# Optimization experiments

Measured on AMD Instinct MI355X. Metric: run time of the kernel, lower is better.

## Reference

```python
import jax, jax.numpy as jnp
import numpy as np

B, S, H, NH = 1, 2048, 2048, 32
HD = H // NH  # 64
DFF = 4 * H
EPS = 1e-5


def layer_norm(x, w, b):
    mu = jnp.mean(x, axis=-1, keepdims=True)
    var = jnp.var(x, axis=-1, keepdims=True)
    return (x - mu) * jax.lax.rsqrt(var + EPS) * w + b


def setup_inputs() -> dict:
    key = jax.random.key(0)
    ks = jax.random.split(key, 16)
    std = 0.02
    hidden_states = jax.random.normal(ks[0], (B, S, H), dtype=jnp.float32)
    # additive causal mask [1,1,S,S]
    causal = jnp.tril(jnp.ones((S, S), dtype=jnp.bool_))
    attention_mask = jnp.where(causal, 0.0, -1e9).astype(jnp.float32)[None, None]
    p = lambda k, shp: (jax.random.normal(k, shp, dtype=jnp.float32) * std)
    return {
        "hidden_states": hidden_states,
        "attention_mask": attention_mask,
        "ln1_w": jnp.ones((H,), jnp.float32), "ln1_b": jnp.zeros((H,), jnp.float32),
        "wq": p(ks[1], (H, H)), "bq": jnp.zeros((H,), jnp.float32),
        "wk": p(ks[2], (H, H)), "bk": jnp.zeros((H,), jnp.float32),
        "wv": p(ks[3], (H, H)), "bv": jnp.zeros((H,), jnp.float32),
        "wo": p(ks[4], (H, H)), "bo": jnp.zeros((H,), jnp.float32),
        "w1": p(ks[5], (H, DFF)), "b1": jnp.zeros((DFF,), jnp.float32),
        "w2": p(ks[6], (DFF, H)), "b2": jnp.zeros((H,), jnp.float32),
        "ln2_w": jnp.ones((H,), jnp.float32), "ln2_b": jnp.zeros((H,), jnp.float32),
    }


def reference(hidden_states, attention_mask, ln1_w, ln1_b, wq, bq, wk, bk, wv, bv,
              wo, bo, w1, b1, w2, b2, ln2_w, ln2_b):
    x = hidden_states
    # --- pre-norm attention ---
    residual = x
    h = layer_norm(x, ln1_w, ln1_b)
    scaling = HD ** -0.5
    q = (h @ wq + bq).reshape(B, S, NH, HD) * scaling
    k = (h @ wk + bk).reshape(B, S, NH, HD)
    v = (h @ wv + bv).reshape(B, S, NH, HD)
    scores = jnp.einsum('bqhd,bkhd->bhqk', q, k) + attention_mask
    p = jax.nn.softmax(scores, axis=-1)  # dropout is identity in eval
    attn = jnp.einsum('bhqk,bkhd->bqhd', p, v).reshape(B, S, H)
    attn = attn @ wo + bo
    x = residual + attn
    # --- pre-norm MLP ---
    residual = x
    h = layer_norm(x, ln2_w, ln2_b)
    h = jax.nn.gelu(h @ w1 + b1, approximate=False) @ w2 + b2
    return residual + h
```

## Files before the change

kernel.cpp:

```cpp
#include <hip/hip_runtime.h>
#include <math.h>

#define H 2048
#define S 2048
#define NH 32
#define HD 64
#define DFF 8192

typedef __attribute__((ext_vector_type(4))) float f32x4;
typedef __attribute__((ext_vector_type(8))) short short8;

static __device__ __forceinline__ ushort f2bf(float f) {
  unsigned u = __float_as_uint(f);
  u += 0x7fff + ((u >> 16) & 1);
  return (ushort)(u >> 16);
}

static __device__ __forceinline__ void gl_lds16(const ushort* g, ushort* l) {
  __builtin_amdgcn_global_load_lds(
      (__attribute__((address_space(1))) const void*)g,
      (__attribute__((address_space(3))) void*)l, 16, 0, 0);
}

__global__ __launch_bounds__(256) void transpose_cast_kernel(
    const float* __restrict__ W, ushort* __restrict__ Wt, int K, int N) {
  __shared__ __align__(16) ushort tile[64][72];
  int n0 = blockIdx.x * 64, k0 = blockIdx.y * 64;
  int t = threadIdx.x;
  int lk = t >> 4;
  int ln4 = (t & 15) * 4;
#pragma unroll
  for (int p = 0; p < 4; p++) {
    int k = p * 16 + lk;
    float4 v = *reinterpret_cast<const float4*>(&W[(size_t)(k0 + k) * N + n0 + ln4]);
    float vv[4] = {v.x, v.y, v.z, v.w};
#pragma unroll
    for (int i = 0; i < 4; i++) {
      int row = ln4 + i;
      int slot = ((k >> 3) ^ (row & 7));
      tile[row][(slot << 3) + (k & 7)] = f2bf(vv[i]);
    }
  }
  __syncthreads();
  int n = t >> 2;
  int kq = (t & 3) * 8;
#pragma unroll
  for (int p = 0; p < 2; p++) {
    int kk = kq + p * 32;
    int slot = ((kk >> 3) ^ (n & 7));
    short8 o = *reinterpret_cast<const short8*>(&tile[n][slot << 3]);
    *reinterpret_cast<short8*>(&Wt[(size_t)(n0 + n) * K + k0 + kk]) = o;
  }
}

__global__ __launch_bounds__(256) void vtrans_kernel(
    const ushort* __restrict__ V, ushort* __restrict__ VT) {
  __shared__ ushort tile[32][33];
  int s0 = blockIdx.x * 32, d0 = blockIdx.y * 32;
  int tx = threadIdx.x & 31, ty = threadIdx.x >> 5;
#pragma unroll
  for (int i = 0; i < 4; i++)
    tile[ty * 4 + i][tx] = V[(size_t)(s0 + ty * 4 + i) * H + d0 + tx];
  __syncthreads();
#pragma unroll
  for (int i = 0; i < 4; i++)
    VT[(size_t)(d0 + ty * 4 + i) * S + s0 + tx] = tile[tx][ty * 4 + i];
}

__global__ __launch_bounds__(256) void biascat_kernel(
    const float* __restrict__ bq, const float* __restrict__ bk,
    const float* __restrict__ bv, float* __restrict__ o) {
  int t = blockIdx.x * 256 + threadIdx.x;
  o[t] = (t < H) ? bq[t] : (t < 2 * H) ? bk[t - H] : bv[t - 2 * H];
}

__global__ __launch_bounds__(256) void ln_kernel(
    const float* __restrict__ x, const float* __restrict__ w,
    const float* __restrict__ b, ushort* __restrict__ out) {
  int row = blockIdx.x, t = threadIdx.x;
  const float4* xr = reinterpret_cast<const float4*>(x + (size_t)row * H);
  float4 v0 = xr[t * 2], v1 = xr[t * 2 + 1];
  float s = v0.x + v0.y + v0.z + v0.w + v1.x + v1.y + v1.z + v1.w;
  float q = v0.x * v0.x + v0.y * v0.y + v0.z * v0.z + v0.w * v0.w +
            v1.x * v1.x + v1.y * v1.y + v1.z * v1.z + v1.w * v1.w;
#pragma unroll
  for (int off = 32; off > 0; off >>= 1) {
    s += __shfl_down(s, off, 64);
    q += __shfl_down(q, off, 64);
  }
  __shared__ float sm[8];
  int lane = t & 63, wv = t >> 6;
  if (lane == 0) { sm[wv] = s; sm[wv + 4] = q; }
  __syncthreads();
  s = sm[0] + sm[1] + sm[2] + sm[3];
  q = sm[4] + sm[5] + sm[6] + sm[7];
  float mu = s * (1.0f / H);
  float var = q * (1.0f / H) - mu * mu;
  float rs = rsqrtf(var + 1e-5f);
  const float4* wr = reinterpret_cast<const float4*>(w);
  const float4* br = reinterpret_cast<const float4*>(b);
  float4 w0 = wr[t * 2], w1v = wr[t * 2 + 1], b0 = br[t * 2], b1v = br[t * 2 + 1];
  short8 pk;
  pk[0] = (short)f2bf((v0.x - mu) * rs * w0.x + b0.x);
  pk[1] = (short)f2bf((v0.y - mu) * rs * w0.y + b0.y);
  pk[2] = (short)f2bf((v0.z - mu) * rs * w0.z + b0.z);
  pk[3] = (short)f2bf((v0.w - mu) * rs * w0.w + b0.w);
  pk[4] = (short)f2bf((v1.x - mu) * rs * w1v.x + b1v.x);
  pk[5] = (short)f2bf((v1.y - mu) * rs * w1v.y + b1v.y);
  pk[6] = (short)f2bf((v1.z - mu) * rs * w1v.z + b1v.z);
  pk[7] = (short)f2bf((v1.w - mu) * rs * w1v.w + b1v.w);
  *reinterpret_cast<short8*>(out + (size_t)row * H + t * 8) = pk;
}

__global__ __launch_bounds__(256) void combine4_kernel(
    const float* __restrict__ res, const float* __restrict__ p0,
    const float* __restrict__ p1, const float* __restrict__ p2,
    const float* __restrict__ p3, const float* __restrict__ bias,
    float* __restrict__ out) {
  size_t i = (size_t)blockIdx.x * 256 + threadIdx.x;
  float4 a = reinterpret_cast<const float4*>(res)[i];
  float4 c0 = reinterpret_cast<const float4*>(p0)[i];
  float4 c1 = reinterpret_cast<const float4*>(p1)[i];
  float4 c2 = reinterpret_cast<const float4*>(p2)[i];
  float4 c3 = reinterpret_cast<const float4*>(p3)[i];
  int col = (int)((i * 4) & (H - 1));
  float4 bb = *reinterpret_cast<const float4*>(bias + col);
  float4 o;
  o.x = a.x + c0.x + c1.x + c2.x + c3.x + bb.x;
  o.y = a.y + c0.y + c1.y + c2.y + c3.y + bb.y;
  o.z = a.z + c0.z + c1.z + c2.z + c3.z + bb.z;
  o.w = a.w + c0.w + c1.w + c2.w + c3.w + bb.w;
  reinterpret_cast<float4*>(out)[i] = o;
}

__global__ __launch_bounds__(256) void combine_ln_kernel(
    const float* __restrict__ res, const float* __restrict__ p0,
    const float* __restrict__ p1, const float* __restrict__ bias,
    const float* __restrict__ lw, const float* __restrict__ lb,
    float* __restrict__ xout, ushort* __restrict__ lnout) {
  int row = blockIdx.x, t = threadIdx.x;
  const float4* rr = reinterpret_cast<const float4*>(res + (size_t)row * H);
  const float4* r0 = reinterpret_cast<const float4*>(p0 + (size_t)row * H);
  const float4* r1 = reinterpret_cast<const float4*>(p1 + (size_t)row * H);
  const float4* bb = reinterpret_cast<const float4*>(bias);
  float4 a0 = rr[t * 2], a1 = rr[t * 2 + 1];
  float4 c0 = r0[t * 2], c1 = r0[t * 2 + 1];
  float4 d0 = r1[t * 2], d1 = r1[t * 2 + 1];
  float4 e0 = bb[t * 2], e1 = bb[t * 2 + 1];
  float4 v0, v1;
  v0.x = a0.x + c0.x + d0.x + e0.x;
  v0.y = a0.y + c0.y + d0.y + e0.y;
  v0.z = a0.z + c0.z + d0.z + e0.z;
  v0.w = a0.w + c0.w + d0.w + e0.w;
  v1.x = a1.x + c1.x + d1.x + e1.x;
  v1.y = a1.y + c1.y + d1.y + e1.y;
  v1.z = a1.z + c1.z + d1.z + e1.z;
  v1.w = a1.w + c1.w + d1.w + e1.w;
  float4* xo = reinterpret_cast<float4*>(xout + (size_t)row * H);
  xo[t * 2] = v0;
  xo[t * 2 + 1] = v1;
  float s = v0.x + v0.y + v0.z + v0.w + v1.x + v1.y + v1.z + v1.w;
  float q = v0.x * v0.x + v0.y * v0.y + v0.z * v0.z + v0.w * v0.w +
            v1.x * v1.x + v1.y * v1.y + v1.z * v1.z + v1.w * v1.w;
#pragma unroll
  for (int off = 32; off > 0; off >>= 1) {
    s += __shfl_down(s, off, 64);
    q += __shfl_down(q, off, 64);
  }
  __shared__ float sm[8];
  int lane = t & 63, wv = t >> 6;
  if (lane == 0) { sm[wv] = s; sm[wv + 4] = q; }
  __syncthreads();
  s = sm[0] + sm[1] + sm[2] + sm[3];
  q = sm[4] + sm[5] + sm[6] + sm[7];
  float mu = s * (1.0f / H);
  float var = q * (1.0f / H) - mu * mu;
  float rs = rsqrtf(var + 1e-5f);
  const float4* wr = reinterpret_cast<const float4*>(lw);
  const float4* br = reinterpret_cast<const float4*>(lb);
  float4 w0 = wr[t * 2], w1v = wr[t * 2 + 1], b0 = br[t * 2], b1v = br[t * 2 + 1];
  short8 pk;
  pk[0] = (short)f2bf((v0.x - mu) * rs * w0.x + b0.x);
  pk[1] = (short)f2bf((v0.y - mu) * rs * w0.y + b0.y);
  pk[2] = (short)f2bf((v0.z - mu) * rs * w0.z + b0.z);
  pk[3] = (short)f2bf((v0.w - mu) * rs * w0.w + b0.w);
  pk[4] = (short)f2bf((v1.x - mu) * rs * w1v.x + b1v.x);
  pk[5] = (short)f2bf((v1.y - mu) * rs * w1v.y + b1v.y);
  pk[6] = (short)f2bf((v1.z - mu) * rs * w1v.z + b1v.z);
  pk[7] = (short)f2bf((v1.w - mu) * rs * w1v.w + b1v.w);
  *reinterpret_cast<short8*>(lnout + (size_t)row * H + t * 8) = pk;
}

template <int MODE>
__global__ __launch_bounds__(512, 2) void gemm256_kernel(
    const ushort* __restrict__ A, const ushort* __restrict__ Bt,
    const float* __restrict__ bias,
    ushort* __restrict__ outb, float* __restrict__ outf,
    int M, int N, int lda, int kbeg, int klen) {
  __shared__ __align__(16) ushort As[2][256 * 64];
  __shared__ __align__(16) ushort Bs[2][256 * 64];
  int tid = threadIdx.x, lane = tid & 63, w = tid >> 6;
  int lm = lane & 15, kg = lane >> 4;
  int wr = w >> 2, wc = w & 3;
  int gx = gridDim.x, nwg = gx * gridDim.y;
  int orig = blockIdx.y * gx + blockIdx.x;
  int wg = (orig & 7) * (nwg >> 3) + (orig >> 3);
  int m0 = (wg % gx) * 256, n0 = (wg / gx) * 256;
  int kb0 = kbeg + blockIdx.z * klen;

  f32x4 acc[8][4] = {};

  const ushort* srcA[4];
  const ushort* srcB[4];
  int dbase[4];
#pragma unroll
  for (int q = 0; q < 4; q++) {
    int g = q * 512 + tid;
    int row = g >> 3, gc = g & 7;
    int col = (gc ^ (row & 7)) << 3;
    srcA[q] = A + (size_t)(m0 + row) * lda + kb0 + col;
    srcB[q] = Bt + (size_t)(n0 + row) * lda + kb0 + col;
    dbase[q] = (q * 512 + w * 64) * 8;
  }

  int nK = klen >> 6;
#pragma unroll
  for (int q = 0; q < 4; q++) gl_lds16(srcA[q], &As[0][dbase[q]]);
#pragma unroll
  for (int q = 0; q < 4; q++) gl_lds16(srcB[q], &Bs[0][dbase[q]]);

  for (int kt = 0; kt < nK; kt++) {
    int cur = kt & 1, nxt = cur ^ 1;
    bool hn = (kt + 1 < nK);
    int ko = (kt + 1) << 6;
    if (hn) {
      gl_lds16(srcA[0] + ko, &As[nxt][dbase[0]]);
      gl_lds16(srcA[1] + ko, &As[nxt][dbase[1]]);
      asm volatile("s_waitcnt vmcnt(2)" ::: "memory");
    } else {
      asm volatile("s_waitcnt vmcnt(0)" ::: "memory");
    }
    __builtin_amdgcn_s_barrier();

    short8 bf[4][2], af[4][2];
#pragma unroll
    for (int n = 0; n < 4; n++)
#pragma unroll
      for (int s = 0; s < 2; s++)
        bf[n][s] = *reinterpret_cast<const short8*>(
            &Bs[cur][(wc * 64 + n * 16 + lm) * 64 + (((s * 4 + kg) ^ (lm & 7)) << 3)]);
#pragma unroll
    for (int i = 0; i < 4; i++)
#pragma unroll
      for (int s = 0; s < 2; s++)
        af[i][s] = *reinterpret_cast<const short8*>(
            &As[cur][(wr * 128 + i * 16 + lm) * 64 + (((s * 4 + kg) ^ (lm & 7)) << 3)]);
    if (hn) {
      gl_lds16(srcA[2] + ko, &As[nxt][dbase[2]]);
      gl_lds16(srcA[3] + ko, &As[nxt][dbase[3]]);
    }
    __builtin_amdgcn_s_barrier();
    __builtin_amdgcn_s_setprio(1);
#pragma unroll
    for (int i = 0; i < 4; i++)
#pragma unroll
      for (int n = 0; n < 2; n++)
#pragma unroll
        for (int s = 0; s < 2; s++)
          acc[i][n] = __builtin_amdgcn_mfma_f32_16x16x32_bf16(af[i][s], bf[n][s], acc[i][n], 0, 0, 0);
    __builtin_amdgcn_s_setprio(0);
    __builtin_amdgcn_s_barrier();

    if (hn) {
      gl_lds16(srcB[0] + ko, &Bs[nxt][dbase[0]]);
      gl_lds16(srcB[1] + ko, &Bs[nxt][dbase[1]]);
    }
    __builtin_amdgcn_s_barrier();
    __builtin_amdgcn_s_setprio(1);
#pragma unroll
    for (int i = 0; i < 4; i++)
#pragma unroll
      for (int n = 2; n < 4; n++)
#pragma unroll
        for (int s = 0; s < 2; s++)
          acc[i][n] = __builtin_amdgcn_mfma_f32_16x16x32_bf16(af[i][s], bf[n][s], acc[i][n], 0, 0, 0);
    __builtin_amdgcn_s_setprio(0);
    __builtin_amdgcn_s_barrier();

#pragma unroll
    for (int i = 0; i < 4; i++)
#pragma unroll
      for (int s = 0; s < 2; s++)
        af[i][s] = *reinterpret_cast<const short8*>(
            &As[cur][(wr * 128 + 64 + i * 16 + lm) * 64 + (((s * 4 + kg) ^ (lm & 7)) << 3)]);
    if (hn) {
      gl_lds16(srcB[2] + ko, &Bs[nxt][dbase[2]]);
      gl_lds16(srcB[3] + ko, &Bs[nxt][dbase[3]]);
    }
    __builtin_amdgcn_s_barrier();
    __builtin_amdgcn_s_setprio(1);
#pragma unroll
    for (int i = 0; i < 4; i++)
#pragma unroll
      for (int n = 0; n < 2; n++)
#pragma unroll
        for (int s = 0; s < 2; s++)
          acc[4 + i][n] = __builtin_amdgcn_mfma_f32_16x16x32_bf16(af[i][s], bf[n][s], acc[4 + i][n], 0, 0, 0);
    __builtin_amdgcn_s_setprio(0);
    __builtin_amdgcn_s_barrier();
    __builtin_amdgcn_s_setprio(1);
#pragma unroll
    for (int i = 0; i < 4; i++)
#pragma unroll
      for (int n = 2; n < 4; n++)
#pragma unroll
        for (int s = 0; s < 2; s++)
          acc[4 + i][n] = __builtin_amdgcn_mfma_f32_16x16x32_bf16(af[i][s], bf[n][s], acc[4 + i][n], 0, 0, 0);
    __builtin_amdgcn_s_setprio(0);
    __builtin_amdgcn_s_barrier();
  }

#pragma unroll
  for (int mi = 0; mi < 8; mi++) {
#pragma unroll
    for (int ni = 0; ni < 4; ni++) {
#pragma unroll
      for (int r = 0; r < 4; r++) {
        int row = m0 + wr * 128 + mi * 16 + kg * 4 + r;
        int col = n0 + wc * 64 + ni * 16 + lm;
        float v = acc[mi][ni][r];
        if (MODE == 0) {
          float t = v + bias[col];
          float sc = (col < H) ? 0.125f : 1.0f;
          size_t idx = (size_t)(col >> 11) * ((size_t)S * H) + (size_t)row * H + (col & (H - 1));
          outb[idx] = f2bf(t * sc);
        } else if (MODE == 1) {
          float t = v + bias[col];
          outb[(size_t)row * N + col] = f2bf(0.5f * t * (1.0f + erff(t * 0.70710678118f)));
        } else {
          int zs = blockIdx.z + ((blockIdx.z >> 1) << 1);
          outf[(size_t)zs * M * N + (size_t)row * N + col] = v;
        }
      }
    }
  }
}

__global__ __launch_bounds__(512) void attn_kernel(
    const ushort* __restrict__ Q, const ushort* __restrict__ Kmat,
    const ushort* __restrict__ VT, ushort* __restrict__ ctx) {
  __shared__ __align__(16) ushort Ks[2][128 * 64];
  __shared__ __align__(16) ushort Vs[2][64 * 128];
  __shared__ __align__(16) ushort Ps[8 * 16 * 64];
  int h = blockIdx.x;
  int x = blockIdx.y;
  int tid = threadIdx.x, lane = tid & 63, w = tid >> 6;
  int lm = lane & 15, kg = lane >> 4;

  int qbA = x, qbB = 15 - x;
  int tA = x + 1;
  const int nt = 17;

  short8 qa[2];
#pragma unroll
  for (int ks = 0; ks < 2; ks++)
    qa[ks] = *reinterpret_cast<const short8*>(
        Q + (size_t)(qbA * 128 + w * 16 + lm) * H + h * 64 + ks * 32 + kg * 8);

  float m_run[4], l_run[4];
  f32x4 o_acc[4] = {};
#pragma unroll
  for (int r = 0; r < 4; r++) { m_run[r] = -1e30f; l_run[r] = 0.f; }

  auto stage = [&](int kb, int buf) {
#pragma unroll
    for (int p = 0; p < 2; p++) {
      int gbase = p * 512 + w * 64;
      int gran = gbase + lane;
      int krow = gran >> 3, gk = gran & 7;
      gl_lds16(Kmat + (size_t)(kb * 128 + krow) * H + h * 64 + ((gk ^ (krow & 7)) << 3),
               &Ks[buf][gbase * 8]);
    }
#pragma unroll
    for (int p = 0; p < 2; p++) {
      int gbase = p * 512 + w * 64;
      int gran = gbase + lane;
      int vrow = gran >> 4, gv = gran & 15;
      gl_lds16(VT + (size_t)(h * 64 + vrow) * S + kb * 128 + ((gv ^ (vrow & 15)) << 3),
               &Vs[buf][gbase * 8]);
    }
  };

  stage(0, 0);
  __syncthreads();

  for (int t = 0; t < nt; t++) {
    int cur = t & 1;
    if (t + 1 < nt) {
      int tn = t + 1;
      stage((tn < tA) ? tn : tn - tA, cur ^ 1);
    }
    bool diag = (t == tA - 1) || (t == nt - 1);

    f32x4 sacc[8] = {};
#pragma unroll
    for (int j = 0; j < 8; j++) {
      int krow = j * 16 + lm;
#pragma unroll
      for (int ks = 0; ks < 2; ks++) {
        short8 kf = *reinterpret_cast<const short8*>(
            &Ks[cur][krow * 64 + (((ks * 4 + kg) ^ (lm & 7)) << 3)]);
        sacc[j] = __builtin_amdgcn_mfma_f32_16x16x32_bf16(qa[ks], kf, sacc[j], 0, 0, 0);
      }
    }
    if (diag) {
#pragma unroll
      for (int j = 0; j < 8; j++)
#pragma unroll
        for (int r = 0; r < 4; r++)
          if (j * 16 + lm > w * 16 + kg * 4 + r) sacc[j][r] = -1e30f;
    }

#pragma unroll
    for (int r = 0; r < 4; r++) {
      float mx = sacc[0][r];
#pragma unroll
      for (int j = 1; j < 8; j++) mx = fmaxf(mx, sacc[j][r]);
      mx = fmaxf(mx, __shfl_xor(mx, 1, 64));
      mx = fmaxf(mx, __shfl_xor(mx, 2, 64));
      mx = fmaxf(mx, __shfl_xor(mx, 4, 64));
      mx = fmaxf(mx, __shfl_xor(mx, 8, 64));
      float mnew = fmaxf(m_run[r], mx);
      float sc = __expf(m_run[r] - mnew);
      m_run[r] = mnew;
      float ps = 0.f;
#pragma unroll
      for (int j = 0; j < 8; j++) {
        float p = __expf(sacc[j][r] - mnew);
        sacc[j][r] = p;
        ps += p;
      }
      ps += __shfl_xor(ps, 1, 64);
      ps += __shfl_xor(ps, 2, 64);
      ps += __shfl_xor(ps, 4, 64);
      ps += __shfl_xor(ps, 8, 64);
      l_run[r] = l_run[r] * sc + ps;
#pragma unroll
      for (int jd = 0; jd < 4; jd++) o_acc[jd][r] *= sc;
    }

#pragma unroll
    for (int c = 0; c < 2; c++) {
#pragma unroll
      for (int jj = 0; jj < 4; jj++)
#pragma unroll
        for (int r = 0; r < 4; r++) {
          int rl = kg * 4 + r;
          int col = jj * 16 + lm;
          Ps[w * 1024 + rl * 64 + (((col >> 3) ^ (rl & 7)) << 3) + (col & 7)] =
              f2bf(sacc[c * 4 + jj][r]);
        }
      short8 pa[2];
#pragma unroll
      for (int ks = 0; ks < 2; ks++)
        pa[ks] = *reinterpret_cast<const short8*>(
            &Ps[w * 1024 + lm * 64 + (((ks * 4 + kg) ^ (lm & 7)) << 3)]);
#pragma unroll
      for (int jd = 0; jd < 4; jd++) {
        int d = jd * 16 + lm;
#pragma unroll
        for (int ks = 0; ks < 2; ks++) {
          short8 vf = *reinterpret_cast<const short8*>(
              &Vs[cur][d * 128 + (((c * 8 + ks * 4 + kg) ^ lm) << 3)]);
          o_acc[jd] = __builtin_amdgcn_mfma_f32_16x16x32_bf16(pa[ks], vf, o_acc[jd], 0, 0, 0);
        }
      }
    }

    if (t == tA - 1) {
#pragma unroll
      for (int jd = 0; jd < 4; jd++)
#pragma unroll
        for (int r = 0; r < 4; r++)
          ctx[(size_t)(qbA * 128 + w * 16 + kg * 4 + r) * H + h * 64 + jd * 16 + lm] =
              f2bf(o_acc[jd][r] / l_run[r]);
#pragma unroll
      for (int r = 0; r < 4; r++) { m_run[r] = -1e30f; l_run[r] = 0.f; }
#pragma unroll
      for (int jd = 0; jd < 4; jd++) o_acc[jd] = f32x4{0.f, 0.f, 0.f, 0.f};
#pragma unroll
      for (int ks = 0; ks < 2; ks++)
        qa[ks] = *reinterpret_cast<const short8*>(
            Q + (size_t)(qbB * 128 + w * 16 + lm) * H + h * 64 + ks * 32 + kg * 8);
    }
    __syncthreads();
  }

#pragma unroll
  for (int jd = 0; jd < 4; jd++)
#pragma unroll
    for (int r = 0; r < 4; r++)
      ctx[(size_t)(qbB * 128 + w * 16 + kg * 4 + r) * H + h * 64 + jd * 16 + lm] =
          f2bf(o_acc[jd][r] / l_run[r]);
}

extern "C" void kernel_launch(void* const* d_in, const int* in_sizes, int n_in,
                              void* d_out, int out_size, void* d_ws, size_t ws_size,
                              hipStream_t stream) {
  const float* x = (const float*)d_in[0];
  const float* ln1w = (const float*)d_in[2];
  const float* ln1b = (const float*)d_in[3];
  const float* wq = (const float*)d_in[4];
  const float* bq = (const float*)d_in[5];
  const float* wk = (const float*)d_in[6];
  const float* bk = (const float*)d_in[7];
  const float* wv = (const float*)d_in[8];
  const float* bv = (const float*)d_in[9];
  const float* wo = (const float*)d_in[10];
  const float* bo = (const float*)d_in[11];
  const float* w1 = (const float*)d_in[12];
  const float* b1 = (const float*)d_in[13];
  const float* w2 = (const float*)d_in[14];
  const float* b2 = (const float*)d_in[15];
  const float* ln2w = (const float*)d_in[16];
  const float* ln2b = (const float*)d_in[17];
  float* out = (float*)d_out;

  char* ws = (char*)d_ws;
  const size_t MB = 1024 * 1024;
  const size_t SH = (size_t)S * H;
  ushort* WT_QKV = (ushort*)(ws);
  ushort* WT_O = (ushort*)(ws + 24 * MB);
  ushort* WT_1 = (ushort*)(ws + 32 * MB);
  ushort* WT_2 = (ushort*)(ws + 64 * MB);
  ushort* LNO = (ushort*)(ws + 96 * MB);
  ushort* QKVB = (ushort*)(ws + 104 * MB);
  ushort* VTb = (ushort*)(ws + 128 * MB);
  ushort* CTX = (ushort*)(ws + 136 * MB);
  float* X1 = (float*)(ws + 144 * MB);
  float* BIASQ = (float*)(ws + 160 * MB);
  ushort* MID = (ushort*)(ws);
  float* SPA = (float*)(ws + 104 * MB);
  float* SPM = (float*)(ws + 32 * MB);

  transpose_cast_kernel<<<dim3(H / 64, H / 64), 256, 0, stream>>>(wq, WT_QKV, H, H);
  transpose_cast_kernel<<<dim3(H / 64, H / 64), 256, 0, stream>>>(wk, WT_QKV + SH, H, H);
  transpose_cast_kernel<<<dim3(H / 64, H / 64), 256, 0, stream>>>(wv, WT_QKV + 2 * SH, H, H);
  transpose_cast_kernel<<<dim3(H / 64, H / 64), 256, 0, stream>>>(wo, WT_O, H, H);
  transpose_cast_kernel<<<dim3(DFF / 64, H / 64), 256, 0, stream>>>(w1, WT_1, H, DFF);
  transpose_cast_kernel<<<dim3(H / 64, DFF / 64), 256, 0, stream>>>(w2, WT_2, DFF, H);
  biascat_kernel<<<3 * H / 256, 256, 0, stream>>>(bq, bk, bv, BIASQ);

  ln_kernel<<<S, 256, 0, stream>>>(x, ln1w, ln1b, LNO);

  gemm256_kernel<0><<<dim3(S / 256, 3 * H / 256), 512, 0, stream>>>(
      LNO, WT_QKV, BIASQ, QKVB, nullptr, S, 3 * H, H, 0, H);

  vtrans_kernel<<<dim3(S / 32, H / 32), 256, 0, stream>>>(QKVB + 2 * SH, VTb);

  attn_kernel<<<dim3(NH, 8), 512, 0, stream>>>(QKVB, QKVB + SH, VTb, CTX);

  gemm256_kernel<3><<<dim3(S / 256, H / 256, 2), 512, 0, stream>>>(
      CTX, WT_O, nullptr, nullptr, SPA, S, H, H, 0, H / 2);
  combine_ln_kernel<<<S, 256, 0, stream>>>(x, SPA, SPA + SH, bo, ln2w, ln2b, X1, LNO);

  gemm256_kernel<1><<<dim3(S / 256, DFF / 256), 512, 0, stream>>>(
      LNO, WT_1, b1, MID, nullptr, S, DFF, H, 0, H);

  gemm256_kernel<3><<<dim3(S / 256, H / 256, 4), 512, 0, stream>>>(
      MID, WT_2, nullptr, nullptr, SPM, S, H, DFF, 0, DFF / 4);
  combine4_kernel<<<SH / 1024, 256, 0, stream>>>(
      X1, SPM, SPM + SH, SPM + 4 * SH, SPM + 5 * SH, b2, out);
}
```

Before: 448.4 us.

## Reschedule GEMM main loop LDS reads and async prefetches per quadrant

Restructures the 256x256 bf16 GEMM inner loop so each k-step splits into four MFMA quadrants. Each quadrant loads only the A/B fragments it needs from LDS, using precomputed base pointers. The async global-to-LDS prefetches for the next tile are interleaved between quadrants, with explicit vmcnt/lgkmcnt waits and sched_barriers, and the first tile is primed before the loop. The goal is to hide LDS and global latency behind MFMA work and cut address arithmetic, at the cost of more barriers and a fragile hand-tuned wait ordering that must match the buffer reuse.

```diff
diff --git a/kernel.cpp b/kernel.cpp
--- a/kernel.cpp
+++ b/kernel.cpp
@@ -223,81 +223,74 @@
     dbase[q] = (q * 512 + w * 64) * 8;
   }
 
+  const ushort* aB0 = &As[0][(wr * 128 + lm) * 64 + ((kg ^ (lm & 7)) << 3)];
+  const ushort* aB1 = &As[0][(wr * 128 + lm) * 64 + (((4 + kg) ^ (lm & 7)) << 3)];
+  const ushort* bB0 = &Bs[0][(wc * 64 + lm) * 64 + ((kg ^ (lm & 7)) << 3)];
+  const ushort* bB1 = &Bs[0][(wc * 64 + lm) * 64 + (((4 + kg) ^ (lm & 7)) << 3)];
+
   int nK = klen >> 6;
-#pragma unroll
-  for (int q = 0; q < 4; q++) gl_lds16(srcA[q], &As[0][dbase[q]]);
-#pragma unroll
-  for (int q = 0; q < 4; q++) gl_lds16(srcB[q], &Bs[0][dbase[q]]);
+  gl_lds16(srcB[0], &Bs[0][dbase[0]]);
+  gl_lds16(srcB[1], &Bs[0][dbase[1]]);
+  gl_lds16(srcB[2], &Bs[0][dbase[2]]);
+  gl_lds16(srcB[3], &Bs[0][dbase[3]]);
+  gl_lds16(srcA[0], &As[0][dbase[0]]);
+  gl_lds16(srcA[2], &As[0][dbase[2]]);
+  gl_lds16(srcA[1], &As[0][dbase[1]]);
+  gl_lds16(srcA[3], &As[0][dbase[3]]);
+  asm volatile("s_waitcnt vmcnt(2)" ::: "memory");
+  __builtin_amdgcn_s_barrier();
 
   for (int kt = 0; kt < nK; kt++) {
     int cur = kt & 1, nxt = cur ^ 1;
     bool hn = (kt + 1 < nK);
     int ko = (kt + 1) << 6;
-    if (hn) {
-      gl_lds16(srcA[0] + ko, &As[nxt][dbase[0]]);
-      gl_lds16(srcA[1] + ko, &As[nxt][dbase[1]]);
-      asm volatile("s_waitcnt vmcnt(2)" ::: "memory");
-    } else {
-      asm volatile("s_waitcnt vmcnt(0)" ::: "memory");
-    }
-    __builtin_amdgcn_s_barrier();
-
-    short8 bf[4][2], af[4][2];
-#pragma unroll
-    for (int n = 0; n < 4; n++)
-#pragma unroll
-      for (int s = 0; s < 2; s++)
-        bf[n][s] = *reinterpret_cast<const short8*>(
-            &Bs[cur][(wc * 64 + n * 16 + lm) * 64 + (((s * 4 + kg) ^ (lm & 7)) << 3)]);
-#pragma unroll
-    for (int i = 0; i < 4; i++)
-#pragma unroll
-      for (int s = 0; s < 2; s++)
-        af[i][s] = *reinterpret_cast<const short8*>(
-            &As[cur][(wr * 128 + i * 16 + lm) * 64 + (((s * 4 + kg) ^ (lm & 7)) << 3)]);
-    if (hn) {
-      gl_lds16(srcA[2] + ko, &As[nxt][dbase[2]]);
-      gl_lds16(srcA[3] + ko, &As[nxt][dbase[3]]);
-    }
-    __builtin_amdgcn_s_barrier();
-    __builtin_amdgcn_s_setprio(1);
-#pragma unroll
-    for (int i = 0; i < 4; i++)
-#pragma unroll
-      for (int n = 0; n < 2; n++)
-#pragma unroll
-        for (int s = 0; s < 2; s++)
-          acc[i][n] = __builtin_amdgcn_mfma_f32_16x16x32_bf16(af[i][s], bf[n][s], acc[i][n], 0, 0, 0);
-    __builtin_amdgcn_s_setprio(0);
-    __builtin_amdgcn_s_barrier();
-
+    const ushort* a0 = aB0 + cur * 16384;
+    const ushort* a1 = aB1 + cur * 16384;
+    const ushort* b0 = bB0 + cur * 16384;
+    const ushort* b1 = bB1 + cur * 16384;
+
+    short8 af[4][2], bf0[2][2], bf1[2][2];
+
+#pragma unroll
+    for (int i = 0; i < 4; i++) {
+      af[i][0] = *reinterpret_cast<const short8*>(a0 + i * 1024);
+      af[i][1] = *reinterpret_cast<const short8*>(a1 + i * 1024);
+    }
+#pragma unroll
+    for (int n = 0; n < 2; n++) {
+      bf0[n][0] = *reinterpret_cast<const short8*>(b0 + n * 1024);
+      bf0[n][1] = *reinterpret_cast<const short8*>(b1 + n * 1024);
+    }
     if (hn) {
       gl_lds16(srcB[0] + ko, &Bs[nxt][dbase[0]]);
       gl_lds16(srcB[1] + ko, &Bs[nxt][dbase[1]]);
     }
     __builtin_amdgcn_s_barrier();
+    asm volatile("s_waitcnt lgkmcnt(0)" ::: "memory");
+    __builtin_amdgcn_sched_barrier(0);
     __builtin_amdgcn_s_setprio(1);
 #pragma unroll
     for (int i = 0; i < 4; i++)
 #pragma unroll
-      for (int n = 2; n < 4; n++)
+      for (int n = 0; n < 2; n++)
 #pragma unroll
         for (int s = 0; s < 2; s++)
-          acc[i][n] = __builtin_amdgcn_mfma_f32_16x16x32_bf16(af[i][s], bf[n][s], acc[i][n], 0, 0, 0);
+          acc[i][n] = __builtin_amdgcn_mfma_f32_16x16x32_bf16(af[i][s], bf0[n][s], acc[i][n], 0, 0, 0);
     __builtin_amdgcn_s_setprio(0);
     __builtin_amdgcn_s_barrier();
 
 #pragma unroll
-    for (int i = 0; i < 4; i++)
-#pragma unroll
-      for (int s = 0; s < 2; s++)
-        af[i][s] = *reinterpret_cast<const short8*>(
-            &As[cur][(wr * 128 + 64 + i * 16 + lm) * 64 + (((s * 4 + kg) ^ (lm & 7)) << 3)]);
+    for (int n = 0; n < 2; n++) {
+      bf1[n][0] = *reinterpret_cast<const short8*>(b0 + 2048 + n * 1024);
+      bf1[n][1] = *reinterpret_cast<const short8*>(b1 + 2048 + n * 1024);
+    }
     if (hn) {
       gl_lds16(srcB[2] + ko, &Bs[nxt][dbase[2]]);
       gl_lds16(srcB[3] + ko, &Bs[nxt][dbase[3]]);
     }
     __builtin_amdgcn_s_barrier();
+    asm volatile("s_waitcnt lgkmcnt(0)" ::: "memory");
+    __builtin_amdgcn_sched_barrier(0);
     __builtin_amdgcn_s_setprio(1);
 #pragma unroll
     for (int i = 0; i < 4; i++)
@@ -305,18 +298,50 @@
       for (int n = 0; n < 2; n++)
 #pragma unroll
         for (int s = 0; s < 2; s++)
-          acc[4 + i][n] = __builtin_amdgcn_mfma_f32_16x16x32_bf16(af[i][s], bf[n][s], acc[4 + i][n], 0, 0, 0);
+          acc[i][2 + n] = __builtin_amdgcn_mfma_f32_16x16x32_bf16(af[i][s], bf1[n][s], acc[i][2 + n], 0, 0, 0);
     __builtin_amdgcn_s_setprio(0);
-    __builtin_amdgcn_s_barrier();
+    if (hn) asm volatile("s_waitcnt vmcnt(4)" ::: "memory");
+    else    asm volatile("s_waitcnt vmcnt(0)" ::: "memory");
+    __builtin_amdgcn_s_barrier();
+
+#pragma unroll
+    for (int i = 0; i < 4; i++) {
+      af[i][0] = *reinterpret_cast<const short8*>(a0 + 4096 + i * 1024);
+      af[i][1] = *reinterpret_cast<const short8*>(a1 + 4096 + i * 1024);
+    }
+    if (hn) {
+      gl_lds16(srcA[0] + ko, &As[nxt][dbase[0]]);
+      gl_lds16(srcA[2] + ko, &As[nxt][dbase[2]]);
+    }
+    __builtin_amdgcn_s_barrier();
+    asm volatile("s_waitcnt lgkmcnt(0)" ::: "memory");
+    __builtin_amdgcn_sched_barrier(0);
     __builtin_amdgcn_s_setprio(1);
 #pragma unroll
     for (int i = 0; i < 4; i++)
 #pragma unroll
-      for (int n = 2; n < 4; n++)
+      for (int n = 0; n < 2; n++)
 #pragma unroll
         for (int s = 0; s < 2; s++)
-          acc[4 + i][n] = __builtin_amdgcn_mfma_f32_16x16x32_bf16(af[i][s], bf[n][s], acc[4 + i][n], 0, 0, 0);
+          acc[4 + i][n] = __builtin_amdgcn_mfma_f32_16x16x32_bf16(af[i][s], bf0[n][s], acc[4 + i][n], 0, 0, 0);
     __builtin_amdgcn_s_setprio(0);
+    __builtin_amdgcn_s_barrier();
+
+    if (hn) {
+      gl_lds16(srcA[1] + ko, &As[nxt][dbase[1]]);
+      gl_lds16(srcA[3] + ko, &As[nxt][dbase[3]]);
+    }
+    __builtin_amdgcn_s_barrier();
+    __builtin_amdgcn_s_setprio(1);
+#pragma unroll
+    for (int i = 0; i < 4; i++)
+#pragma unroll
+      for (int n = 0; n < 2; n++)
+#pragma unroll
+        for (int s = 0; s < 2; s++)
+          acc[4 + i][2 + n] = __builtin_amdgcn_mfma_f32_16x16x32_bf16(af[i][s], bf1[n][s], acc[4 + i][2 + n], 0, 0, 0);
+    __builtin_amdgcn_s_setprio(0);
+    if (hn) asm volatile("s_waitcnt vmcnt(2)" ::: "memory");
     __builtin_amdgcn_s_barrier();
   }
 
```

Result: faster. 427.4 us (-4.7%).
